# Kernel optimization log

Measured on AMD Instinct MI355X. Metric: run time of the kernel, lower is better.

The kernel has to match this reference:

```python
import jax, jax.numpy as jnp
import numpy as np

GUMBEL_BETA = 0.0036  # gumbel_beta init kwarg
N1, N2, BOX_DIM = 160, 1024, 256


def _center_sigmoid_offsets(data):
    # CenterSigmoidBoxTensor: softplus with beta=10, then sigmoid
    sp = jax.nn.softplus(10.0 * data[..., 1, :]) / 10.0
    zmin = jax.nn.sigmoid(data[..., 0, :] - sp)
    zmax = jax.nn.sigmoid(data[..., 0, :] + sp)
    return zmin, zmax


def setup_inputs() -> dict:
    key = jax.random.key(0)
    k1, k2 = jax.random.split(key)
    box1s = jax.random.normal(k1, (N1, 2, BOX_DIM), dtype=jnp.float32)
    box2s = jax.random.normal(k2, (N2, 2, BOX_DIM), dtype=jnp.float32)
    return {"box1s": box1s, "box2s": box2s}


def reference(box1s, box2s):
    gb = GUMBEL_BETA
    z1, Z1 = _center_sigmoid_offsets(box1s)  # [N1, D]
    z2, Z2 = _center_sigmoid_offsets(box2s)  # [N2, D]

    # Pairwise: i over box2s (outer), j over box1s (inner) -> [N2, N1, D]
    a, b = z2[:, None, :], z1[None, :, :]
    # gb * logsumexp([a/gb, b/gb], 0) == max(a,b) + gb*log1p(exp(-|a-b|/gb))
    lse_min = jnp.maximum(a, b) + gb * jnp.log1p(jnp.exp(-jnp.abs(a - b) / gb))
    inter_min = jnp.maximum(lse_min, jnp.maximum(a, b))

    A, B = Z2[:, None, :], Z1[None, :, :]
    # -gb * logsumexp([-A/gb, -B/gb], 0) == min(A,B) - gb*log1p(exp(-|A-B|/gb))
    lse_max = jnp.minimum(A, B) - gb * jnp.log1p(jnp.exp(-jnp.abs(A - B) / gb))
    inter_max = jnp.minimum(lse_max, jnp.minimum(A, B))

    n2, n1, d = inter_min.shape
    return inter_min.reshape(n2 * n1, d), inter_max.reshape(n2 * n1, d)
```

## Files before the change

kernel.cpp:

```cpp
#include <hip/hip_runtime.h>
#include <hip/hip_bf16.h>

#define BN1 160
#define BN2 1024
#define BD  256

#define GB_F     0.0036f
#define INV_GB_F (1.0f / 0.0036f)

__device__ float g_z1min[BN1 * BD];
__device__ float g_z1max[BN1 * BD];
__device__ float g_z2min[BN2 * BD];
__device__ float g_z2max[BN2 * BD];

__device__ __forceinline__ float softplus10(float x) {
    float y = 10.0f * x;
    float t = __expf(-fabsf(y));
    return (fmaxf(y, 0.0f) + __logf(1.0f + t)) * 0.1f;
}

__device__ __forceinline__ float sigmoidf(float x) {
    return 1.0f / (1.0f + __expf(-x));
}

__global__ __launch_bounds__(256) void precompute_kernel(
        const float* __restrict__ box1s, const float* __restrict__ box2s) {
    int idx = blockIdx.x * 256 + threadIdx.x;
    if (idx < BN2 * BD) {
        int n = idx >> 8;
        int d = idx & (BD - 1);
        float c  = box2s[n * 2 * BD + d];
        float sp = softplus10(box2s[n * 2 * BD + BD + d]);
        g_z2min[idx] = sigmoidf(c - sp);
        g_z2max[idx] = sigmoidf(c + sp);
    } else {
        int j = idx - BN2 * BD;
        if (j < BN1 * BD) {
            int n = j >> 8;
            int d = j & (BD - 1);
            float c  = box1s[n * 2 * BD + d];
            float sp = softplus10(box1s[n * 2 * BD + BD + d]);
            g_z1min[j] = sigmoidf(c - sp);
            g_z1max[j] = sigmoidf(c + sp);
        }
    }
}

union F4 {
    float4 v;
    float f[4];
};

__global__ __launch_bounds__(256) void pairs_kernel(float* __restrict__ out) {
    const int t    = threadIdx.x;
    const int row  = blockIdx.x * 4 + (t >> 6);
    const int d0   = (t & 63) << 2;

    const int i2 = row / BN1;
    const int i1 = row - i2 * BN1;

    F4 a, A, b, B;
    a.v = *(const float4*)(g_z2min + i2 * BD + d0);
    A.v = *(const float4*)(g_z2max + i2 * BD + d0);
    b.v = *(const float4*)(g_z1min + i1 * BD + d0);
    B.v = *(const float4*)(g_z1max + i1 * BD + d0);

    F4 o0, o1;
#pragma unroll
    for (int j = 0; j < 4; ++j) {
        float av = a.f[j], bv = b.f[j];
        float m  = fmaxf(av, bv);
        float c0 = GB_F * __logf(1.0f + __expf(-fabsf(av - bv) * INV_GB_F));
        o0.f[j]  = fmaxf(m + c0, m);

        float Av = A.f[j], Bv = B.f[j];
        float M  = fminf(Av, Bv);
        float c1 = GB_F * __logf(1.0f + __expf(-fabsf(Av - Bv) * INV_GB_F));
        o1.f[j]  = fminf(M - c1, M);
    }

    const size_t base = (size_t)row * BD + d0;
    const size_t half = (size_t)BN2 * BN1 * BD;
    *(float4*)(out + base)        = o0.v;
    *(float4*)(out + half + base) = o1.v;
}

extern "C" void kernel_launch(void* const* d_in, const int* in_sizes, int n_in,
                              void* d_out, int out_size, void* d_ws, size_t ws_size,
                              hipStream_t stream) {
    const float* box1s = (const float*)d_in[0];
    const float* box2s = (const float*)d_in[1];
    float* out = (float*)d_out;

    precompute_kernel<<<1184, 256, 0, stream>>>(box1s, box2s);

    pairs_kernel<<<(BN2 * BN1) / 4, 256, 0, stream>>>(out);
}
```

Measured before the change: 326.0 us.

## Tile pairs kernel over box2 rows and use nontemporal output stores

Each wave now keeps its box1 row in registers and loops over 16 box2 rows, so there are fewer blocks and fewer loads per output. Output writes use nontemporal stores so the large streaming output does not pollute the caches. The kernel is write-bandwidth bound, with about 335 MB of output. Fewer blocks means less parallelism, and the write ordering changes from contiguous per block to strided by BN1 rows.

```diff
diff --git a/kernel.cpp b/kernel.cpp
--- a/kernel.cpp
+++ b/kernel.cpp
@@ -4,9 +4,13 @@
 #define BN1 160
 #define BN2 1024
 #define BD  256
+#define TI2 16
+#define RI1 4
 
 #define GB_F     0.0036f
 #define INV_GB_F (1.0f / 0.0036f)
+
+typedef float f32x4 __attribute__((ext_vector_type(4)));
 
 __device__ float g_z1min[BN1 * BD];
 __device__ float g_z1max[BN1 * BD];
@@ -47,42 +51,51 @@
 }
 
 union F4 {
-    float4 v;
+    f32x4 v;
     float f[4];
 };
 
 __global__ __launch_bounds__(256) void pairs_kernel(float* __restrict__ out) {
     const int t    = threadIdx.x;
-    const int row  = blockIdx.x * 4 + (t >> 6);
-    const int d0   = (t & 63) << 2;
+    const int wave = t >> 6;
+    const int lane = t & 63;
+    const int d0   = lane << 2;
 
-    const int i2 = row / BN1;
-    const int i1 = row - i2 * BN1;
+    const int nTile2  = BN2 / TI2;
+    const int i1      = (blockIdx.x / nTile2) * RI1 + wave;
+    const int i2base  = (blockIdx.x % nTile2) * TI2;
 
-    F4 a, A, b, B;
-    a.v = *(const float4*)(g_z2min + i2 * BD + d0);
-    A.v = *(const float4*)(g_z2max + i2 * BD + d0);
-    b.v = *(const float4*)(g_z1min + i1 * BD + d0);
-    B.v = *(const float4*)(g_z1max + i1 * BD + d0);
+    F4 b, B;
+    b.v = *(const f32x4*)(g_z1min + i1 * BD + d0);
+    B.v = *(const f32x4*)(g_z1max + i1 * BD + d0);
 
-    F4 o0, o1;
+    const size_t half = (size_t)BN2 * BN1 * BD;
+
+#pragma unroll 4
+    for (int k = 0; k < TI2; ++k) {
+        const int i2 = i2base + k;
+        F4 a, A;
+        a.v = *(const f32x4*)(g_z2min + i2 * BD + d0);
+        A.v = *(const f32x4*)(g_z2max + i2 * BD + d0);
+
+        F4 o0, o1;
 #pragma unroll
-    for (int j = 0; j < 4; ++j) {
-        float av = a.f[j], bv = b.f[j];
-        float m  = fmaxf(av, bv);
-        float c0 = GB_F * __logf(1.0f + __expf(-fabsf(av - bv) * INV_GB_F));
-        o0.f[j]  = fmaxf(m + c0, m);
+        for (int j = 0; j < 4; ++j) {
+            float av = a.f[j], bv = b.f[j];
+            float m  = fmaxf(av, bv);
+            float c0 = GB_F * __logf(1.0f + __expf(-fabsf(av - bv) * INV_GB_F));
+            o0.f[j]  = fmaxf(m + c0, m);
 
-        float Av = A.f[j], Bv = B.f[j];
-        float M  = fminf(Av, Bv);
-        float c1 = GB_F * __logf(1.0f + __expf(-fabsf(Av - Bv) * INV_GB_F));
-        o1.f[j]  = fminf(M - c1, M);
+            float Av = A.f[j], Bv = B.f[j];
+            float M  = fminf(Av, Bv);
+            float c1 = GB_F * __logf(1.0f + __expf(-fabsf(Av - Bv) * INV_GB_F));
+            o1.f[j]  = fminf(M - c1, M);
+        }
+
+        const size_t base = ((size_t)i2 * BN1 + i1) * BD + d0;
+        __builtin_nontemporal_store(o0.v, (f32x4*)(out + base));
+        __builtin_nontemporal_store(o1.v, (f32x4*)(out + half + base));
     }
-
-    const size_t base = (size_t)row * BD + d0;
-    const size_t half = (size_t)BN2 * BN1 * BD;
-    *(float4*)(out + base)        = o0.v;
-    *(float4*)(out + half + base) = o1.v;
 }
 
 extern "C" void kernel_launch(void* const* d_in, const int* in_sizes, int n_in,
@@ -94,5 +107,5 @@
 
     precompute_kernel<<<1184, 256, 0, stream>>>(box1s, box2s);
 
-    pairs_kernel<<<(BN2 * BN1) / 4, 256, 0, stream>>>(out);
+    pairs_kernel<<<(BN1 / RI1) * (BN2 / TI2), 256, 0, stream>>>(out);
 }
```

After: 341.8 us. 1.05x slower.
